# Performance work log

Measured on AMD Instinct MI355X. Metric: run time of the kernel, lower is better.

The kernel has to match this reference:

```python
import jax, jax.numpy as jnp
import numpy as np

N_HEADS = 16

def setup_inputs() -> dict:
    key = jax.random.key(0)
    k1, k2, k3 = jax.random.split(key, 3)
    B, T, C = 4, 2048, 1024
    x = jax.random.normal(k1, (B, T, C), dtype=jnp.float32)
    w_qkv = jax.random.normal(k2, (C, 3 * C), dtype=jnp.float32) * (1.0 / np.sqrt(C))
    w_out = jax.random.normal(k3, (C, C), dtype=jnp.float32) * (1.0 / np.sqrt(C))
    return {"x": x, "w_qkv": w_qkv, "w_out": w_out}

def reference(x, w_qkv, w_out):
    B, T, C = x.shape
    H = N_HEADS
    D = C // H
    qkv = jnp.einsum('btc,cf->btf', x, w_qkv).reshape(B, T, 3, H, D)
    q, k, v = qkv[:, :, 0], qkv[:, :, 1], qkv[:, :, 2]  # [B,T,H,D]
    q = q.transpose(0, 2, 1, 3)  # [B,H,T,D]
    k = k.transpose(0, 2, 1, 3)
    v = v.transpose(0, 2, 1, 3)
    scale = 1.0 / jnp.sqrt(jnp.asarray(D, dtype=x.dtype))
    scores = jnp.einsum('bhqd,bhkd->bhqk', q, k) * scale  # [B,H,T,T]
    causal = jnp.tril(jnp.ones((T, T), dtype=bool))
    scores = jnp.where(causal[None, None], scores, jnp.asarray(-jnp.inf, dtype=scores.dtype))
    attn = jax.nn.softmax(scores, axis=-1)
    ctx = jnp.einsum('bhqk,bhkd->bhqd', attn, v)  # [B,H,T,D]
    ctx = ctx.transpose(0, 2, 1, 3).reshape(B, T, C)
    return jnp.einsum('btc,co->bto', ctx, w_out)
```

## Files before the change

kernel.cpp:

```cpp
#include <hip/hip_runtime.h>

typedef __attribute__((ext_vector_type(8))) short bf16x8;
typedef __attribute__((ext_vector_type(4))) short bf16x4;
typedef __attribute__((ext_vector_type(4))) float f32x4;
typedef __attribute__((ext_vector_type(4))) unsigned short u16x4;

#define MFMA16(a, b, c) __builtin_amdgcn_mfma_f32_16x16x32_bf16((a), (b), (c), 0, 0, 0)
#define MFMA16K16(a, b, c) __builtin_amdgcn_mfma_f32_16x16x16bf16_1k((a), (b), (c), 0, 0, 0)

__device__ __forceinline__ unsigned short f2bf(float f) {
    union { float f; unsigned int u; } x; x.f = f;
    unsigned int r = x.u + 0x7FFFu + ((x.u >> 16) & 1u);
    return (unsigned short)(r >> 16);
}
__device__ __forceinline__ unsigned int fbits(float f) {
    union { float f; unsigned int u; } x; x.f = f;
    return x.u;
}
__device__ __forceinline__ void gload_lds16(const void* g, void* l) {
    __builtin_amdgcn_global_load_lds(
        (const __attribute__((address_space(1))) unsigned int*)g,
        (__attribute__((address_space(3))) unsigned int*)l,
        16, 0, 0);
}

__global__ void cast_x(const float* __restrict__ in, unsigned short* __restrict__ hi,
                       int n) {
    int i = (blockIdx.x * blockDim.x + threadIdx.x) * 4;
    if (i >= n) return;
    float4 v = *(const float4*)(in + i);
    float vv[4] = {v.x, v.y, v.z, v.w};
    u16x4 h;
#pragma unroll
    for (int j = 0; j < 4; ++j) h[j] = f2bf(vv[j]);
    *(u16x4*)(hi + i) = h;
}

__global__ void tcast_k(const float* __restrict__ in, unsigned short* __restrict__ out,
                        int K, int N) {
    __shared__ float tile[64][65];
    int n0 = blockIdx.x * 64, k0 = blockIdx.y * 64;
    for (int i = threadIdx.x; i < 4096; i += 256) {
        int r = i >> 6, c = i & 63;
        tile[r][c] = in[(size_t)(k0 + r) * N + n0 + c];
    }
    __syncthreads();
    for (int i = threadIdx.x; i < 4096; i += 256) {
        int r = i >> 6, c = i & 63;
        out[(size_t)(n0 + r) * K + k0 + c] = f2bf(tile[c][r]);
    }
}

__global__ __launch_bounds__(256, 4) void gemm_qkv(
    const unsigned short* __restrict__ A,
    const unsigned short* __restrict__ Bt,
    unsigned short* __restrict__ qout, unsigned short* __restrict__ kout,
    unsigned short* __restrict__ vtout) {
    const int K = 1024;
    __shared__ __align__(16) unsigned short smem[17408];
    unsigned short* sA = smem;
    unsigned short* sB = smem + 8192;
    int tid = threadIdx.x, lane = tid & 63, w = tid >> 6;
    int c = lane & 15, quad = lane >> 4;
    int sw = c & 7;
    int wm = (w >> 1) * 64, wn = (w & 1) * 64;

    int wg = blockIdx.y * 24 + blockIdx.x;
    int nid = (wg & 7) * 192 + (wg >> 3);
    int m_blk = nid / 24, n_blk = nid - m_blk * 24;
    int m0 = m_blk * 128, n0 = n_blk * 128;

    f32x4 acc[4][4];
#pragma unroll
    for (int i = 0; i < 4; i++)
#pragma unroll
        for (int j = 0; j < 4; j++) acc[i][j] = (f32x4){0.f, 0.f, 0.f, 0.f};

    for (int kk = 0; kk < K; kk += 64) {
#pragma unroll
        for (int p = 0; p < 4; ++p) {
            int ch = p * 256 + tid;
            int r = ch >> 3;
            int gs = (ch & 7) ^ (r & 7);
            gload_lds16(A + (size_t)(m0 + r) * K + kk + gs * 8, &sA[ch * 8]);
            gload_lds16(Bt + (size_t)(n0 + r) * K + kk + gs * 8, &sB[ch * 8]);
        }
        __syncthreads();
#pragma unroll
        for (int ks8 = 0; ks8 < 8; ks8 += 4) {
            bf16x8 af[4], bfr[4];
#pragma unroll
            for (int mt = 0; mt < 4; ++mt)
                af[mt] = *(const bf16x8*)&sA[(wm + mt * 16 + c) * 64 +
                                             ((ks8 + quad) ^ sw) * 8];
#pragma unroll
            for (int nt = 0; nt < 4; ++nt)
                bfr[nt] = *(const bf16x8*)&sB[(wn + nt * 16 + c) * 64 +
                                              ((ks8 + quad) ^ sw) * 8];
#pragma unroll
            for (int mt = 0; mt < 4; ++mt)
#pragma unroll
                for (int nt = 0; nt < 4; ++nt)
                    acc[mt][nt] = MFMA16(af[mt], bfr[nt], acc[mt][nt]);
        }
        __syncthreads();
    }

    const float QSCALE = 0.1803368801111601f;
    bool vreg = (n0 >= 2048);
    if (!vreg) {
        float scale = (n0 < 1024) ? QSCALE : 1.0f;
#pragma unroll
        for (int mt = 0; mt < 4; ++mt)
#pragma unroll
            for (int nt = 0; nt < 4; ++nt)
#pragma unroll
                for (int r = 0; r < 4; ++r)
                    smem[(wm + mt * 16 + quad * 4 + r) * 136 + wn + nt * 16 + c] =
                        f2bf(acc[mt][nt][r] * scale);
    } else {
#pragma unroll
        for (int mt = 0; mt < 4; ++mt)
#pragma unroll
            for (int nt = 0; nt < 4; ++nt)
#pragma unroll
                for (int r = 0; r < 4; ++r)
                    smem[(wn + nt * 16 + c) * 136 + wm + mt * 16 + quad * 4 + r] =
                        f2bf(acc[mt][nt][r]);
    }
    __syncthreads();

    int rr = tid >> 4, cc = tid & 15;
    if (!vreg) {
        int col = n0 + cc * 8;
        int which = col >> 10;
        int h = (col >> 6) & 15, d = col & 63;
        unsigned short* dst = which ? kout : qout;
#pragma unroll
        for (int j = 0; j < 8; ++j) {
            int row = rr + j * 16;
            int grow = m0 + row;
            int b = grow >> 11, t = grow & 2047;
            size_t bh_ = (size_t)(b * 16 + h);
            bf16x8 vv = *(const bf16x8*)&smem[row * 136 + cc * 8];
            *(bf16x8*)&dst[(bh_ * 2048 + t) * 64 + d] = vv;
        }
    } else {
        int grow = m0 + cc * 8;
        int b = grow >> 11, t = grow & 2047;
#pragma unroll
        for (int j = 0; j < 8; ++j) {
            int nrow = rr + j * 16;
            int col = n0 + nrow;
            int h = (col >> 6) & 15, d = col & 63;
            size_t bh_ = (size_t)(b * 16 + h);
            bf16x8 vv = *(const bf16x8*)&smem[nrow * 136 + cc * 8];
            *(bf16x8*)&vtout[(bh_ * 64 + d) * 2048 + t] = vv;
        }
    }
}

__global__ __launch_bounds__(256, 2) void gemm2_bt(
    const unsigned short* __restrict__ A,
    const unsigned short* __restrict__ Bt,
    float* __restrict__ out) {
    const int K = 1024, N = 1024;
    __shared__ __align__(16) unsigned short sA[128 * 64], sB[128 * 64];
    int tid = threadIdx.x, lane = tid & 63, w = tid >> 6;
    int c = lane & 15, quad = lane >> 4;
    int sw = c & 7;
    int wm = (w >> 1) * 64, wn = (w & 1) * 64;

    int wg = blockIdx.y * 8 + blockIdx.x;
    int nid = (wg & 7) * 64 + (wg >> 3);
    int m_blk = nid >> 3, n_blk = nid & 7;
    int m0 = m_blk * 128, n0 = n_blk * 128;

    f32x4 acc[4][4];
#pragma unroll
    for (int i = 0; i < 4; i++)
#pragma unroll
        for (int j = 0; j < 4; j++) acc[i][j] = (f32x4){0.f, 0.f, 0.f, 0.f};

    for (int kk = 0; kk < K; kk += 64) {
#pragma unroll
        for (int p = 0; p < 4; ++p) {
            int ch = p * 256 + tid;
            int r = ch >> 3;
            int gs = (ch & 7) ^ (r & 7);
            gload_lds16(A + (size_t)(m0 + r) * K + kk + gs * 8, &sA[ch * 8]);
            gload_lds16(Bt + (size_t)(n0 + r) * K + kk + gs * 8, &sB[ch * 8]);
        }
        __syncthreads();
#pragma unroll
        for (int ks8 = 0; ks8 < 8; ks8 += 4) {
            bf16x8 af[4], bfr[4];
#pragma unroll
            for (int mt = 0; mt < 4; ++mt)
                af[mt] = *(const bf16x8*)&sA[(wm + mt * 16 + c) * 64 +
                                             ((ks8 + quad) ^ sw) * 8];
#pragma unroll
            for (int nt = 0; nt < 4; ++nt)
                bfr[nt] = *(const bf16x8*)&sB[(wn + nt * 16 + c) * 64 +
                                              ((ks8 + quad) ^ sw) * 8];
#pragma unroll
            for (int mt = 0; mt < 4; ++mt)
#pragma unroll
                for (int nt = 0; nt < 4; ++nt)
                    acc[mt][nt] = MFMA16(af[mt], bfr[nt], acc[mt][nt]);
        }
        __syncthreads();
    }

#pragma unroll
    for (int mt = 0; mt < 4; ++mt)
#pragma unroll
        for (int nt = 0; nt < 4; ++nt)
#pragma unroll
            for (int r = 0; r < 4; ++r) {
                int row = m0 + wm + mt * 16 + quad * 4 + r;
                int col = n0 + wn + nt * 16 + c;
                out[(size_t)row * N + col] = acc[mt][nt][r];
            }
}

#define SSTR 72
__device__ const int JOB_ORDER[24] = {7, 15, 23, 14, 22, 6,  13, 21, 12, 20, 5,  11,
                                      19, 10, 18, 4,  9,  17, 8,  16, 3,  2,  1,  0};

__global__ __launch_bounds__(256, 4) void attn_k(
    const unsigned short* __restrict__ q,
    const unsigned short* __restrict__ k,
    const unsigned short* __restrict__ vt,
    unsigned short* __restrict__ ctx,
    float* __restrict__ op, float* __restrict__ lbuf) {
    const int T = 2048, D = 64;
    __shared__ __align__(16) unsigned short sK[2][64 * SSTR];
    __shared__ __align__(16) unsigned short sV[2][64 * SSTR];

    int tid = threadIdx.x, lane = tid & 63, w = tid >> 6;
    int c = lane & 15, quad = lane >> 4;

    int rank = blockIdx.x >> 6, bh = blockIdx.x & 63;
    int t = JOB_ORDER[rank];
    int jt, kt0, nkt;
    bool split, has_diag;
    if (t < 8)        { jt = t;     kt0 = 0;      nkt = 2 * t + 2; split = false; has_diag = true; }
    else if (t < 16)  { jt = t;     kt0 = 0;      nkt = jt + 1;    split = true;  has_diag = false; }
    else              { jt = t - 8; kt0 = jt + 1; nkt = jt + 1;    split = true;  has_diag = true; }
    int kt_end = kt0 + nkt;
    int b = bh >> 4, hh = bh & 15;

    const unsigned short* qh = q + (size_t)bh * T * D;
    const unsigned short* kh = k + (size_t)bh * T * D;
    const unsigned short* vh = vt + (size_t)bh * D * T;

    int dv = tid >> 3, tcv = (tid & 7) * 8;
    int q0 = jt * 128;
    int qloc = w * 16 + c;
    int qrow[2];
    qrow[0] = q0 + qloc;
    qrow[1] = qrow[0] + 64;

    bf16x8 bq[2][2];
#pragma unroll
    for (int g = 0; g < 2; ++g) {
        bq[g][0] = *(const bf16x8*)&qh[(size_t)qrow[g] * D + quad * 8];
        bq[g][1] = *(const bf16x8*)&qh[(size_t)qrow[g] * D + 32 + quad * 8];
    }

    f32x4 o[2][4];
#pragma unroll
    for (int g = 0; g < 2; ++g)
#pragma unroll
        for (int nt = 0; nt < 4; ++nt) o[g][nt] = (f32x4){0.f, 0.f, 0.f, 0.f};
    float l_i[2] = {0.f, 0.f};

    int kb0 = kt0 * 64;
    bf16x8 kr0 = *(const bf16x8*)&kh[(size_t)(kb0 + lane) * D + w * 8];
    bf16x8 kr1 = *(const bf16x8*)&kh[(size_t)(kb0 + lane) * D + w * 8 + 32];
    bf16x8 vr0 = *(const bf16x8*)&vh[(size_t)dv * T + kb0 + tcv];
    bf16x8 vr1 = *(const bf16x8*)&vh[(size_t)(dv + 32) * T + kb0 + tcv];
    *(bf16x8*)&sK[0][lane * SSTR + w * 8] = kr0;
    *(bf16x8*)&sK[0][lane * SSTR + w * 8 + 32] = kr1;
    *(bf16x8*)&sV[0][dv * SSTR + tcv] = vr0;
    *(bf16x8*)&sV[0][(dv + 32) * SSTR + tcv] = vr1;
    __syncthreads();

    int cur = 0;
    for (int kt = kt0; kt < kt_end; ++kt) {
        int kb = kt * 64;
        if (kt + 1 < kt_end) {
            int kb2 = kb + 64;
            kr0 = *(const bf16x8*)&kh[(size_t)(kb2 + lane) * D + w * 8];
            kr1 = *(const bf16x8*)&kh[(size_t)(kb2 + lane) * D + w * 8 + 32];
            vr0 = *(const bf16x8*)&vh[(size_t)dv * T + kb2 + tcv];
            vr1 = *(const bf16x8*)&vh[(size_t)(dv + 32) * T + kb2 + tcv];
        }
        bool g0_active = !has_diag || (kt != 2 * jt + 1);

        const unsigned short* sKc = sK[cur];
        const unsigned short* sVc = sV[cur];

        f32x4 st[2][4];
        __builtin_amdgcn_s_setprio(1);
#pragma unroll
        for (int mt = 0; mt < 4; ++mt) {
            bf16x8 ak0 = *(const bf16x8*)&sKc[(mt * 16 + c) * SSTR + quad * 8];
            bf16x8 ak1 = *(const bf16x8*)&sKc[(mt * 16 + c) * SSTR + 32 + quad * 8];
#pragma unroll
            for (int g = 0; g < 2; ++g) {
                f32x4 z = (f32x4){0.f, 0.f, 0.f, 0.f};
                z = MFMA16(ak0, bq[g][0], z);
                z = MFMA16(ak1, bq[g][1], z);
                st[g][mt] = z;
            }
        }
        __builtin_amdgcn_s_setprio(0);

        bf16x4 pf[2][4];
#pragma unroll
        for (int g = 0; g < 2; ++g) {
            if (g == 0 && !g0_active) continue;
            bool diag = has_diag && (kb == q0 + (g << 6));
            if (diag) {
#pragma unroll
                for (int mt = 0; mt < 4; ++mt)
#pragma unroll
                    for (int r = 0; r < 4; ++r)
                        if (mt * 16 + quad * 4 + r > qloc) st[g][mt][r] = -1.0e30f;
            }
            float rs = 0.f;
#pragma unroll
            for (int mt = 0; mt < 4; ++mt) {
                float p0 = __builtin_exp2f(st[g][mt][0]);
                float p1 = __builtin_exp2f(st[g][mt][1]);
                float p2 = __builtin_exp2f(st[g][mt][2]);
                float p3 = __builtin_exp2f(st[g][mt][3]);
                rs += (p0 + p1) + (p2 + p3);
                unsigned int w0 = __builtin_amdgcn_perm(
                    fbits(p1) + 0x8000u, fbits(p0) + 0x8000u, 0x07060302u);
                unsigned int w1 = __builtin_amdgcn_perm(
                    fbits(p3) + 0x8000u, fbits(p2) + 0x8000u, 0x07060302u);
                uint2 pk; pk.x = w0; pk.y = w1;
                pf[g][mt] = *(bf16x4*)&pk;
            }
            l_i[g] += rs;
        }

        __builtin_amdgcn_s_setprio(1);
#pragma unroll
        for (int mt = 0; mt < 4; ++mt) {
#pragma unroll
            for (int nt = 0; nt < 4; ++nt) {
                bf16x4 av = *(const bf16x4*)&sVc[(nt * 16 + c) * SSTR + mt * 16 + quad * 4];
                if (g0_active) o[0][nt] = MFMA16K16(av, pf[0][mt], o[0][nt]);
                o[1][nt] = MFMA16K16(av, pf[1][mt], o[1][nt]);
            }
        }
        __builtin_amdgcn_s_setprio(0);

        if (kt + 1 < kt_end) {
            int nxt = cur ^ 1;
            *(bf16x8*)&sK[nxt][lane * SSTR + w * 8] = kr0;
            *(bf16x8*)&sK[nxt][lane * SSTR + w * 8 + 32] = kr1;
            *(bf16x8*)&sV[nxt][dv * SSTR + tcv] = vr0;
            *(bf16x8*)&sV[nxt][(dv + 32) * SSTR + tcv] = vr1;
            __syncthreads();
            cur = nxt;
        }
    }

    if (!split) {
#pragma unroll
        for (int g = 0; g < 2; ++g) {
            float l = l_i[g];
            l += __shfl_xor(l, 16);
            l += __shfl_xor(l, 32);
            float inv = 1.0f / l;
#pragma unroll
            for (int nt = 0; nt < 4; ++nt) {
                u16x4 ob;
#pragma unroll
                for (int r = 0; r < 4; ++r) ob[r] = f2bf(o[g][nt][r] * inv);
                *(u16x4*)&ctx[(size_t)(b * T + qrow[g]) * 1024 + hh * 64 + nt * 16 + quad * 4] = ob;
            }
        }
    } else {
        int piece = has_diag ? 1 : 0;
        int sidx = bh * 8 + (jt - 8);
        size_t base = (size_t)(piece * 512 + sidx) * 128;
#pragma unroll
        for (int g = 0; g < 2; ++g) {
            float l = l_i[g];
            l += __shfl_xor(l, 16);
            l += __shfl_xor(l, 32);
            int rloc = qrow[g] - q0;
            if (quad == 0) lbuf[base + rloc] = l;
            float* orow = op + (base + rloc) * 64;
#pragma unroll
            for (int nt = 0; nt < 4; ++nt)
                *(f32x4*)&orow[nt * 16 + quad * 4] = o[g][nt];
        }
    }
}

__global__ void merge_k(const float* __restrict__ op, const float* __restrict__ lbuf,
                        unsigned short* __restrict__ ctx) {
    int gid = blockIdx.x * 256 + threadIdx.x;
    int row = gid >> 4, dq = (gid & 15) * 4;
    int sidx = row >> 7, rloc = row & 127;
    int bh = sidx >> 3, jt = 8 + (sidx & 7);
    int b = bh >> 4, hh = bh & 15;
    int tq = jt * 128 + rloc;
    float inv = 1.0f / (lbuf[row] + lbuf[65536 + row]);
    float4 o0 = *(const float4*)(op + (size_t)row * 64 + dq);
    float4 o1 = *(const float4*)(op + (size_t)(65536 + row) * 64 + dq);
    u16x4 ob;
    ob[0] = f2bf((o0.x + o1.x) * inv);
    ob[1] = f2bf((o0.y + o1.y) * inv);
    ob[2] = f2bf((o0.z + o1.z) * inv);
    ob[3] = f2bf((o0.w + o1.w) * inv);
    *(u16x4*)&ctx[((size_t)(b * 2048 + tq)) * 1024 + hh * 64 + dq] = ob;
}

extern "C" void kernel_launch(void* const* d_in, const int* in_sizes, int n_in,
                              void* d_out, int out_size, void* d_ws, size_t ws_size,
                              hipStream_t stream) {
    const float* x     = (const float*)d_in[0];
    const float* w_qkv = (const float*)d_in[1];
    const float* w_out = (const float*)d_in[2];
    float* out = (float*)d_out;

    char* ws = (char*)d_ws;
    unsigned short* wqkvt = (unsigned short*)(ws + 0);
    unsigned short* woutt = (unsigned short*)(ws + 6291456);
    unsigned short* x_bf  = (unsigned short*)(ws + 8388608);
    unsigned short* qb    = (unsigned short*)(ws + 25165824);
    unsigned short* kb    = (unsigned short*)(ws + 41943040);
    unsigned short* vtb   = (unsigned short*)(ws + 58720256);
    unsigned short* ctx   = (unsigned short*)(ws + 8388608);

    float* op   = (float*)d_out;
    float* lbuf = (float*)ws;

    cast_x<<<8192, 256, 0, stream>>>(x, x_bf, 8388608);
    tcast_k<<<dim3(48, 16), 256, 0, stream>>>(w_qkv, wqkvt, 1024, 3072);
    tcast_k<<<dim3(16, 16), 256, 0, stream>>>(w_out, woutt, 1024, 1024);
    gemm_qkv<<<dim3(24, 64), 256, 0, stream>>>(x_bf, wqkvt, qb, kb, vtb);
    attn_k<<<1536, 256, 0, stream>>>(qb, kb, vtb, ctx, op, lbuf);
    merge_k<<<4096, 256, 0, stream>>>(op, lbuf, ctx);
    gemm2_bt<<<dim3(8, 64), 256, 0, stream>>>(ctx, woutt, out);
}
```

Measured before the change: 262.7 us.

## Single-buffer attention LDS tiles for higher occupancy and fuse weight transpose casts

The attention kernel drops its double-buffered K/V shared-memory tiles in favour of single buffers, adding a second barrier before each overwrite, and raises its launch-bounds occupancy target from 4 to 6 blocks. This halves LDS use per block so more blocks can be resident and hide latency. The cost is an extra __syncthreads per key tile and tighter register limits that may cause spills. Separately, the two weight transpose-cast launches are merged into one kernel to save a launch.

```diff
diff --git a/kernel.cpp b/kernel.cpp
--- a/kernel.cpp
+++ b/kernel.cpp
@@ -36,10 +36,17 @@
     *(u16x4*)(hi + i) = h;
 }
 
-__global__ void tcast_k(const float* __restrict__ in, unsigned short* __restrict__ out,
-                        int K, int N) {
+__global__ void tcast_k2(const float* __restrict__ wqkv, unsigned short* __restrict__ wqkvt,
+                         const float* __restrict__ wout, unsigned short* __restrict__ woutt) {
     __shared__ float tile[64][65];
-    int n0 = blockIdx.x * 64, k0 = blockIdx.y * 64;
+    const int K = 1024;
+    int bx = blockIdx.x;
+    const float* in;
+    unsigned short* out;
+    int N, n0;
+    if (bx < 48) { in = wqkv; out = wqkvt; N = 3072; n0 = bx * 64; }
+    else         { in = wout; out = woutt; N = 1024; n0 = (bx - 48) * 64; }
+    int k0 = blockIdx.y * 64;
     for (int i = threadIdx.x; i < 4096; i += 256) {
         int r = i >> 6, c = i & 63;
         tile[r][c] = in[(size_t)(k0 + r) * N + n0 + c];
@@ -228,15 +235,15 @@
 __device__ const int JOB_ORDER[24] = {7, 15, 23, 14, 22, 6,  13, 21, 12, 20, 5,  11,
                                       19, 10, 18, 4,  9,  17, 8,  16, 3,  2,  1,  0};
 
-__global__ __launch_bounds__(256, 4) void attn_k(
+__global__ __launch_bounds__(256, 6) void attn_k(
     const unsigned short* __restrict__ q,
     const unsigned short* __restrict__ k,
     const unsigned short* __restrict__ vt,
     unsigned short* __restrict__ ctx,
     float* __restrict__ op, float* __restrict__ lbuf) {
     const int T = 2048, D = 64;
-    __shared__ __align__(16) unsigned short sK[2][64 * SSTR];
-    __shared__ __align__(16) unsigned short sV[2][64 * SSTR];
+    __shared__ __align__(16) unsigned short sK[64 * SSTR];
+    __shared__ __align__(16) unsigned short sV[64 * SSTR];
 
     int tid = threadIdx.x, lane = tid & 63, w = tid >> 6;
     int c = lane & 15, quad = lane >> 4;
@@ -281,13 +288,12 @@
     bf16x8 kr1 = *(const bf16x8*)&kh[(size_t)(kb0 + lane) * D + w * 8 + 32];
     bf16x8 vr0 = *(const bf16x8*)&vh[(size_t)dv * T + kb0 + tcv];
     bf16x8 vr1 = *(const bf16x8*)&vh[(size_t)(dv + 32) * T + kb0 + tcv];
-    *(bf16x8*)&sK[0][lane * SSTR + w * 8] = kr0;
-    *(bf16x8*)&sK[0][lane * SSTR + w * 8 + 32] = kr1;
-    *(bf16x8*)&sV[0][dv * SSTR + tcv] = vr0;
-    *(bf16x8*)&sV[0][(dv + 32) * SSTR + tcv] = vr1;
+    *(bf16x8*)&sK[lane * SSTR + w * 8] = kr0;
+    *(bf16x8*)&sK[lane * SSTR + w * 8 + 32] = kr1;
+    *(bf16x8*)&sV[dv * SSTR + tcv] = vr0;
+    *(bf16x8*)&sV[(dv + 32) * SSTR + tcv] = vr1;
     __syncthreads();
 
-    int cur = 0;
     for (int kt = kt0; kt < kt_end; ++kt) {
         int kb = kt * 64;
         if (kt + 1 < kt_end) {
@@ -299,15 +305,12 @@
         }
         bool g0_active = !has_diag || (kt != 2 * jt + 1);
 
-        const unsigned short* sKc = sK[cur];
-        const unsigned short* sVc = sV[cur];
-
         f32x4 st[2][4];
         __builtin_amdgcn_s_setprio(1);
 #pragma unroll
         for (int mt = 0; mt < 4; ++mt) {
-            bf16x8 ak0 = *(const bf16x8*)&sKc[(mt * 16 + c) * SSTR + quad * 8];
-            bf16x8 ak1 = *(const bf16x8*)&sKc[(mt * 16 + c) * SSTR + 32 + quad * 8];
+            bf16x8 ak0 = *(const bf16x8*)&sK[(mt * 16 + c) * SSTR + quad * 8];
+            bf16x8 ak1 = *(const bf16x8*)&sK[(mt * 16 + c) * SSTR + 32 + quad * 8];
 #pragma unroll
             for (int g = 0; g < 2; ++g) {
                 f32x4 z = (f32x4){0.f, 0.f, 0.f, 0.f};
@@ -353,7 +356,7 @@
         for (int mt = 0; mt < 4; ++mt) {
 #pragma unroll
             for (int nt = 0; nt < 4; ++nt) {
-                bf16x4 av = *(const bf16x4*)&sVc[(nt * 16 + c) * SSTR + mt * 16 + quad * 4];
+                bf16x4 av = *(const bf16x4*)&sV[(nt * 16 + c) * SSTR + mt * 16 + quad * 4];
                 if (g0_active) o[0][nt] = MFMA16K16(av, pf[0][mt], o[0][nt]);
                 o[1][nt] = MFMA16K16(av, pf[1][mt], o[1][nt]);
             }
@@ -361,13 +364,12 @@
         __builtin_amdgcn_s_setprio(0);
 
         if (kt + 1 < kt_end) {
-            int nxt = cur ^ 1;
-            *(bf16x8*)&sK[nxt][lane * SSTR + w * 8] = kr0;
-            *(bf16x8*)&sK[nxt][lane * SSTR + w * 8 + 32] = kr1;
-            *(bf16x8*)&sV[nxt][dv * SSTR + tcv] = vr0;
-            *(bf16x8*)&sV[nxt][(dv + 32) * SSTR + tcv] = vr1;
             __syncthreads();
-            cur = nxt;
+            *(bf16x8*)&sK[lane * SSTR + w * 8] = kr0;
+            *(bf16x8*)&sK[lane * SSTR + w * 8 + 32] = kr1;
+            *(bf16x8*)&sV[dv * SSTR + tcv] = vr0;
+            *(bf16x8*)&sV[(dv + 32) * SSTR + tcv] = vr1;
+            __syncthreads();
         }
     }
 
@@ -445,8 +447,7 @@
     float* lbuf = (float*)ws;
 
     cast_x<<<8192, 256, 0, stream>>>(x, x_bf, 8388608);
-    tcast_k<<<dim3(48, 16), 256, 0, stream>>>(w_qkv, wqkvt, 1024, 3072);
-    tcast_k<<<dim3(16, 16), 256, 0, stream>>>(w_out, woutt, 1024, 1024);
+    tcast_k2<<<dim3(64, 16), 256, 0, stream>>>(w_qkv, wqkvt, w_out, woutt);
     gemm_qkv<<<dim3(24, 64), 256, 0, stream>>>(x_bf, wqkvt, qb, kb, vtb);
     attn_k<<<1536, 256, 0, stream>>>(qb, kb, vtb, ctx, op, lbuf);
     merge_k<<<4096, 256, 0, stream>>>(op, lbuf, ctx);
```

Result: slower. 531.6 us (+102.4%).
